# Optimization experiments

Measured on AMD Instinct MI355X. Metric: run time of the kernel, lower is better.

## Reference

```python
import jax, jax.numpy as jnp
import numpy as np

K_MASK = jnp.finfo(jnp.bfloat16).min
ROPE_THETA = 1000000.0


def _rope_sincos(position_ids, head_dim, theta):
    # position_ids: [b, t] int -> sin, cos: [b, t, head_dim//2]
    frac = jnp.arange(0, head_dim, 2, dtype=jnp.float32) / head_dim
    timescale = theta ** frac
    ang = position_ids[..., None].astype(jnp.float32) / timescale
    return jnp.sin(ang), jnp.cos(ang)


def _apply_rope(x, sin, cos):
    # x: [b, t, n, h]; sin/cos: [b, t, h//2]
    h = x.shape[-1]
    x1, x2 = x[..., : h // 2], x[..., h // 2 :]
    s = sin[:, :, None, :]
    c = cos[:, :, None, :]
    return jnp.concatenate([x1 * c - x2 * s, x2 * c + x1 * s], axis=-1).astype(x.dtype)


def setup_inputs() -> dict:
    key = jax.random.key(0)
    ks = jax.random.split(key, 8)
    b, t, S = 8, 16, 8192
    D, N, K, H = 1536, 12, 2, 128
    std = 0.01  # nnx.initializers.normal() default stddev
    return {
        "x": jax.random.normal(ks[0], (b, t, D), jnp.float32),
        "k_cache": jax.random.normal(ks[1], (b, S, K, H), jnp.float32),
        "v_cache": jax.random.normal(ks[2], (b, S, K, H), jnp.float32),
        "wq": jax.random.normal(ks[3], (D, N, H), jnp.float32) * std,
        "bq": jnp.zeros((N, H), jnp.float32),
        "wk": jax.random.normal(ks[4], (D, K, H), jnp.float32) * std,
        "bk": jnp.zeros((K, H), jnp.float32),
        "wv": jax.random.normal(ks[5], (D, K, H), jnp.float32) * std,
        "bv": jnp.zeros((K, H), jnp.float32),
        "wo": jax.random.normal(ks[6], (N, H, D), jnp.float32) * std,
        "segment_ids": jnp.ones((b, t), jnp.int32),
        "start_ind": jnp.zeros((8,), jnp.int32),
        "cur_ind": 4096,
    }


def reference(x, k_cache, v_cache, wq, bq, wk, bk, wv, bv, wo,
              segment_ids, start_ind, cur_ind):
    b, t, D = x.shape
    S = k_cache.shape[1]
    N, H = wq.shape[1], wq.shape[2]
    K = wk.shape[1]
    G = N // K  # n_rep
    scale = H ** -0.5

    # projections with bias
    q = jnp.einsum("btd,dnh->btnh", x, wq) + bq
    kp = jnp.einsum("btd,dkh->btkh", x, wk) + bk
    v = jnp.einsum("btd,dkh->btkh", x, wv) + bv

    # left-pad bookkeeping (count_left_pads) and start index resolution
    nonpad = segment_ids != 0  # [b, t]
    left_pads = jnp.argmax(nonpad, axis=-1).astype(jnp.int32)
    start = jnp.where(start_ind < 0, left_pads, start_ind)  # [b]

    # positions from segment ids, offset by current cache index
    positions = jnp.maximum(jnp.cumsum(nonpad.astype(jnp.int32), axis=-1) - 1, 0) + cur_ind
    sin, cos = _rope_sincos(positions, H, ROPE_THETA)
    q = _apply_rope(q, sin, cos)
    kp = _apply_rope(kp, sin, cos)

    # cache update
    k_cache = jax.lax.dynamic_update_slice(k_cache, kp.astype(k_cache.dtype), (0, cur_ind, 0, 0))
    v_cache = jax.lax.dynamic_update_slice(v_cache, v.astype(v_cache.dtype), (0, cur_ind, 0, 0))

    # GQA attention over full cache
    qg = q.reshape(b, t, K, G, H)
    logits = jnp.einsum("btkgh,bskh->btskg", qg, k_cache) * scale  # [b,t,S,K,G]

    q_pos = cur_ind + jnp.arange(t, dtype=jnp.int32)[None, :] - start[:, None]  # [b,t]
    ts = jnp.arange(S, dtype=jnp.int32)
    kv_seg = (ts[None, :] >= start[:, None]) & (ts[None, :] < cur_ind + t)  # [b,S]
    k_pos = ts[None, :] - start[:, None]
    causal = k_pos[:, None, :] <= q_pos[:, :, None]  # [b,t,S]
    seg = kv_seg[:, None, :].astype(segment_ids.dtype) == segment_ids[:, :, None]  # [b,t,S]
    mask = (causal & seg)[:, :, :, None, None]

    logits = jnp.where(mask, logits, K_MASK)
    w = jax.nn.softmax(logits.astype(jnp.float32), axis=2).astype(logits.dtype)
    qkv = jnp.einsum("btskg,bskh->btkgh", w, v_cache).reshape(b, t, N, H)
    return jnp.einsum("btnh,nhd->btd", qkv, wo)
```

## Files before the change

### kernel.cpp

```cpp
#include <hip/hip_runtime.h>
#include <hip/hip_bf16.h>

#define B_ 8
#define T_ 16
#define D_ 1536
#define N_ 12
#define KH_ 2
#define G_ 6
#define H_ 128
#define S_ 8192
#define NCHUNK 16
#define SPLITS 8

typedef __attribute__((ext_vector_type(8))) short bf16x8;
typedef __attribute__((ext_vector_type(4))) float f32x4;
typedef __attribute__((ext_vector_type(4))) unsigned short u16x4;

__device__ __forceinline__ unsigned short f2bf(float x) {
    unsigned u = __float_as_uint(x);
    u += 0x7fffu + ((u >> 16) & 1u);
    return (unsigned short)(u >> 16);
}
__device__ __forceinline__ float bf2f(unsigned short h) {
    return __uint_as_float(((unsigned)h) << 16);
}

__global__ __launch_bounds__(256, 4) void gemm_splitk(
    const float* __restrict__ A,
    const float* __restrict__ W0, int n0, int ldb0,
    const float* __restrict__ W1, int n1, int ldb1,
    const float* __restrict__ W2, int ldb2,
    float* __restrict__ part, int NTOT, int Kdim)
{
    __shared__ __align__(16) unsigned short Ah[64][40], Al[64][40];
    __shared__ __align__(16) unsigned short Bh[64][40], Bl[64][40];
    const int tid = threadIdx.x;
    const int wave = tid >> 6, lane = tid & 63;
    const int col = lane & 15, g = lane >> 4;
    const int row0 = blockIdx.y * 64;
    const int c0 = blockIdx.x * 64;
    const int ks = Kdim / gridDim.z;
    const int k0 = blockIdx.z * ks;

    const float* Bp; int ldb, bc0;
    if (c0 < n0)           { Bp = W0; ldb = ldb0; bc0 = c0; }
    else if (c0 < n0 + n1) { Bp = W1; ldb = ldb1; bc0 = c0 - n0; }
    else                   { Bp = W2; ldb = ldb2; bc0 = c0 - n0 - n1; }

    f32x4 acc[4];
#pragma unroll
    for (int nt = 0; nt < 4; ++nt) acc[nt] = (f32x4){0.f, 0.f, 0.f, 0.f};

    for (int kk = 0; kk < ks; kk += 32) {
        __syncthreads();
        if (tid < 128) {
#pragma unroll
            for (int c = tid; c < 512; c += 128) {
                int r = c >> 3, k4 = c & 7;
                float4 v = *(const float4*)&A[(size_t)(row0 + r) * Kdim + k0 + kk + k4 * 4];
                float f[4] = {v.x, v.y, v.z, v.w};
                u16x4 hv, lv;
#pragma unroll
                for (int i = 0; i < 4; ++i) {
                    unsigned short hh = f2bf(f[i]);
                    hv[i] = hh; lv[i] = f2bf(f[i] - bf2f(hh));
                }
                *(u16x4*)&Ah[r][k4 * 4] = hv;
                *(u16x4*)&Al[r][k4 * 4] = lv;
            }
        } else {
            int t2 = tid - 128;
            int kq = t2 >> 4, cq = t2 & 15;
            float a[4][4];
#pragma unroll
            for (int r = 0; r < 4; ++r) {
                float4 v = *(const float4*)&Bp[(size_t)(k0 + kk + kq * 4 + r) * ldb + bc0 + cq * 4];
                a[r][0] = v.x; a[r][1] = v.y; a[r][2] = v.z; a[r][3] = v.w;
            }
#pragma unroll
            for (int cc = 0; cc < 4; ++cc) {
                u16x4 hv, lv;
#pragma unroll
                for (int r = 0; r < 4; ++r) {
                    unsigned short hh = f2bf(a[r][cc]);
                    hv[r] = hh; lv[r] = f2bf(a[r][cc] - bf2f(hh));
                }
                *(u16x4*)&Bh[cq * 4 + cc][kq * 4] = hv;
                *(u16x4*)&Bl[cq * 4 + cc][kq * 4] = lv;
            }
        }
        __syncthreads();

        bf16x8 ah = *(const bf16x8*)&Ah[wave * 16 + col][g * 8];
        bf16x8 al = *(const bf16x8*)&Al[wave * 16 + col][g * 8];
#pragma unroll
        for (int nt = 0; nt < 4; ++nt) {
            bf16x8 bh = *(const bf16x8*)&Bh[nt * 16 + col][g * 8];
            bf16x8 bl = *(const bf16x8*)&Bl[nt * 16 + col][g * 8];
            acc[nt] = __builtin_amdgcn_mfma_f32_16x16x32_bf16(ah, bh, acc[nt], 0, 0, 0);
            acc[nt] = __builtin_amdgcn_mfma_f32_16x16x32_bf16(ah, bl, acc[nt], 0, 0, 0);
            acc[nt] = __builtin_amdgcn_mfma_f32_16x16x32_bf16(al, bh, acc[nt], 0, 0, 0);
        }
    }
#pragma unroll
    for (int nt = 0; nt < 4; ++nt)
#pragma unroll
        for (int j = 0; j < 4; ++j) {
            size_t prow = (size_t)blockIdx.z * 128 + row0 + wave * 16 + g * 4 + j;
            part[prow * NTOT + c0 + nt * 16 + col] = acc[nt][j];
        }
}

__global__ __launch_bounds__(256) void rope_reduce(
    const float* __restrict__ part,
    const float* __restrict__ bq, const float* __restrict__ bk,
    const float* __restrict__ bv,
    const int* __restrict__ seg, const int* __restrict__ curp,
    float* __restrict__ q_rope, float* __restrict__ k_new,
    float* __restrict__ v_new)
{
    const int row = blockIdx.x;
    const int b = row >> 4, t = row & 15;
    const int tid = threadIdx.x;
    __shared__ float S[2048];
    __shared__ float sc[64][2];

    const int CUR = curp[0];
    int c = 0;
    for (int tt = 0; tt <= t; ++tt) c += (seg[b * T_ + tt] != 0) ? 1 : 0;
    int pos = max(c - 1, 0) + CUR;

    if (tid < 64) {
        float frac = (2.0f * tid) / (float)H_;
        float ts = expf(frac * logf(1000000.0f));
        float ang = (float)pos / ts;
        sc[tid][0] = sinf(ang);
        sc[tid][1] = cosf(ang);
    }
    for (int e = tid; e < 2048; e += 256) {
        float s = 0.f;
#pragma unroll
        for (int sp = 0; sp < SPLITS; ++sp)
            s += part[((size_t)sp * 128 + row) * 2048 + e];
        S[e] = s;
    }
    __syncthreads();

    for (int e = tid; e < 768; e += 256) {
        int n = e >> 6, i = e & 63;
        float x1 = S[n * 128 + i] + bq[n * 128 + i];
        float x2 = S[n * 128 + i + 64] + bq[n * 128 + i + 64];
        float s = sc[i][0], co = sc[i][1];
        q_rope[(size_t)row * 1536 + n * 128 + i]      = x1 * co - x2 * s;
        q_rope[(size_t)row * 1536 + n * 128 + i + 64] = x2 * co + x1 * s;
    }
    if (tid < 128) {
        int n = tid >> 6, i = tid & 63;
        float x1 = S[1536 + n * 128 + i] + bk[n * 128 + i];
        float x2 = S[1536 + n * 128 + i + 64] + bk[n * 128 + i + 64];
        float s = sc[i][0], co = sc[i][1];
        k_new[(size_t)row * 256 + n * 128 + i]      = x1 * co - x2 * s;
        k_new[(size_t)row * 256 + n * 128 + i + 64] = x2 * co + x1 * s;
    }
    v_new[(size_t)row * 256 + tid] = S[1792 + tid] + bv[tid];
}

__global__ __launch_bounds__(384) void attn_mfma(
    const float* __restrict__ q_rope, const float* __restrict__ k_new,
    const float* __restrict__ v_new,
    const float* __restrict__ k_cache, const float* __restrict__ v_cache,
    const int* __restrict__ seg, const int* __restrict__ start_ind,
    const int* __restrict__ curp,
    float* __restrict__ part)
{
    const int chunk = blockIdx.x, b = blockIdx.y, kh = blockIdx.z;
    const int tid = threadIdx.x;
    const int wave = tid >> 6, lane = tid & 63;
    const int col = lane & 15, g = lane >> 4;
    const float scale = 0.088388347648318447f;
    const float NEG_INF = -__builtin_inff();

    const int CUR = curp[0];
    const int SPAN = CUR + T_;
    const int CH = (SPAN + NCHUNK - 1) / NCHUNK;
    const int s0 = chunk * CH;
    const int s1 = min(s0 + CH, SPAN);

    int st = start_ind[b];
    if (st < 0) {
        st = 0;
        for (int tt = 0; tt < T_; ++tt)
            if (seg[b * T_ + tt] != 0) { st = tt; break; }
    }

    __shared__ __align__(16) unsigned short Vt[6][128][32];
    __shared__ __align__(16) unsigned short Pl[6][16][40];

    const int qbase = wave * 16;
    const int qi_a = qbase + col;
    const int t_a = (qi_a * 171) >> 10;
    const int gh_a = qi_a - t_a * G_;
    const float* qp = &q_rope[(((size_t)b * T_ + t_a) * N_ + kh * G_ + gh_a) * H_];
    bf16x8 qh[4], ql[4];
#pragma unroll
    for (int ks = 0; ks < 4; ++ks) {
        float4 va = *(const float4*)&qp[ks * 32 + g * 8];
        float4 vb = *(const float4*)&qp[ks * 32 + g * 8 + 4];
        float f[8] = {va.x, va.y, va.z, va.w, vb.x, vb.y, vb.z, vb.w};
#pragma unroll
        for (int i = 0; i < 8; ++i) {
            float xs = f[i] * scale;
            unsigned short hh = f2bf(xs);
            qh[ks][i] = (short)hh;
            ql[ks][i] = (short)f2bf(xs - bf2f(hh));
        }
    }

    int qpos_r[4], segid_r[4];
#pragma unroll
    for (int j = 0; j < 4; ++j) {
        int qi_c = qbase + g * 4 + j;
        int t_c = (qi_c * 171) >> 10;
        segid_r[j] = seg[b * T_ + t_c];
        qpos_r[j] = CUR + t_c - st;
    }

    float m[4], lsum[4];
#pragma unroll
    for (int j = 0; j < 4; ++j) { m[j] = NEG_INF; lsum[j] = 0.f; }
    f32x4 oacc[8];
#pragma unroll
    for (int nt = 0; nt < 8; ++nt) oacc[nt] = (f32x4){0.f, 0.f, 0.f, 0.f};

    auto krow = [&](int s) -> const float* {
        s = min(s, SPAN - 1);
        return (s < CUR)
            ? &k_cache[((((size_t)b * S_ + s) * KH_) + kh) * H_]
            : &k_new[((((size_t)b * T_ + (s - CUR)) * KH_) + kh) * H_];
    };
    auto vrow = [&](int s) -> const float* {
        s = min(s, SPAN - 1);
        return (s < CUR)
            ? &v_cache[((((size_t)b * S_ + s) * KH_) + kh) * H_]
            : &v_new[((((size_t)b * T_ + (s - CUR)) * KH_) + kh) * H_];
    };

    auto loadK = [&](float4* kf, int stile) {
#pragma unroll
        for (int kt = 0; kt < 2; ++kt) {
            const float* kr = krow(stile + kt * 16 + col);
#pragma unroll
            for (int ks = 0; ks < 4; ++ks) {
                kf[kt * 8 + ks * 2 + 0] = *(const float4*)(kr + ks * 32 + g * 8);
                kf[kt * 8 + ks * 2 + 1] = *(const float4*)(kr + ks * 32 + g * 8 + 4);
            }
        }
    };
    auto loadV = [&](float4* vf, int stile) {
#pragma unroll
        for (int r = 0; r < 8; ++r) {
            const float* vr = vrow(stile + g * 8 + r);
            vf[r * 2 + 0] = *(const float4*)(vr + col * 8);
            vf[r * 2 + 1] = *(const float4*)(vr + col * 8 + 4);
        }
    };

    const int ntiles = (s1 - s0 + 31) >> 5;
    float4 kf[16], vf[16];
    loadK(kf, s0);

    for (int ti = 0; ti < ntiles; ++ti) {
        const int stile = s0 + ti * 32;
        loadV(vf, stile);

        f32x4 sacc0 = {0.f, 0.f, 0.f, 0.f}, sacc1 = {0.f, 0.f, 0.f, 0.f};
#pragma unroll
        for (int kt = 0; kt < 2; ++kt) {
#pragma unroll
            for (int ks = 0; ks < 4; ++ks) {
                float4 a = kf[kt * 8 + ks * 2], bb = kf[kt * 8 + ks * 2 + 1];
                float f[8] = {a.x, a.y, a.z, a.w, bb.x, bb.y, bb.z, bb.w};
                union { bf16x8 v; __hip_bfloat162 h2[4]; } Hh, Ll;
#pragma unroll
                for (int i = 0; i < 4; ++i) {
                    float2 p = make_float2(f[2 * i], f[2 * i + 1]);
                    Hh.h2[i] = __float22bfloat162_rn(p);
                    float2 q = __bfloat1622float2(Hh.h2[i]);
                    Ll.h2[i] = __float22bfloat162_rn(make_float2(p.x - q.x, p.y - q.y));
                }
                if (kt == 0) {
                    sacc0 = __builtin_amdgcn_mfma_f32_16x16x32_bf16(qh[ks], Hh.v, sacc0, 0, 0, 0);
                    sacc0 = __builtin_amdgcn_mfma_f32_16x16x32_bf16(ql[ks], Hh.v, sacc0, 0, 0, 0);
                    sacc0 = __builtin_amdgcn_mfma_f32_16x16x32_bf16(qh[ks], Ll.v, sacc0, 0, 0, 0);
                } else {
                    sacc1 = __builtin_amdgcn_mfma_f32_16x16x32_bf16(qh[ks], Hh.v, sacc1, 0, 0, 0);
                    sacc1 = __builtin_amdgcn_mfma_f32_16x16x32_bf16(ql[ks], Hh.v, sacc1, 0, 0, 0);
                    sacc1 = __builtin_amdgcn_mfma_f32_16x16x32_bf16(qh[ks], Ll.v, sacc1, 0, 0, 0);
                }
            }
        }

        if (ti + 1 < ntiles) loadK(kf, stile + 32);

        float rj[4];
        const int skey0 = stile + col, skey1 = stile + 16 + col;
#pragma unroll
        for (int j = 0; j < 4; ++j) {
            bool v0 = (skey0 < s1) && (skey0 - st <= qpos_r[j]) &&
                      (((skey0 >= st) ? 1 : 0) == segid_r[j]);
            bool v1 = (skey1 < s1) && (skey1 - st <= qpos_r[j]) &&
                      (((skey1 >= st) ? 1 : 0) == segid_r[j]);
            float lg0 = v0 ? sacc0[j] : NEG_INF;
            float lg1 = v1 ? sacc1[j] : NEG_INF;
            float tm = fmaxf(lg0, lg1);
            tm = fmaxf(tm, __shfl_xor(tm, 1));
            tm = fmaxf(tm, __shfl_xor(tm, 2));
            tm = fmaxf(tm, __shfl_xor(tm, 4));
            tm = fmaxf(tm, __shfl_xor(tm, 8));
            float mn = fmaxf(m[j], tm);
            float r, p0, p1;
            if (mn == NEG_INF) { r = 1.f; p0 = 0.f; p1 = 0.f; }
            else {
                r  = __expf(m[j] - mn);
                p0 = __expf(lg0 - mn);
                p1 = __expf(lg1 - mn);
            }
            float ps = p0 + p1;
            ps += __shfl_xor(ps, 1);
            ps += __shfl_xor(ps, 2);
            ps += __shfl_xor(ps, 4);
            ps += __shfl_xor(ps, 8);
            lsum[j] = lsum[j] * r + ps;
            m[j] = mn;
            rj[j] = r;
            int row = g * 4 + j;
            Pl[wave][row][col]      = f2bf(p0);
            Pl[wave][row][16 + col] = f2bf(p1);
        }

#pragma unroll
        for (int nt = 0; nt < 8; ++nt) {
#pragma unroll
            for (int j = 0; j < 4; ++j) oacc[nt][j] *= rj[j];
        }

#pragma unroll
        for (int c = 0; c < 8; ++c) {
            float fr[8];
#pragma unroll
            for (int r = 0; r < 8; ++r)
                fr[r] = ((const float*)&vf[r * 2 + (c >> 2)])[c & 3];
            union { bf16x8 v; __hip_bfloat162 h2[4]; } W;
#pragma unroll
            for (int i = 0; i < 4; ++i)
                W.h2[i] = __float22bfloat162_rn(make_float2(fr[2 * i], fr[2 * i + 1]));
            *(bf16x8*)&Vt[wave][(c << 4) | col][g * 8] = W.v;
        }

        bf16x8 pa = *(const bf16x8*)&Pl[wave][col][g * 8];
#pragma unroll
        for (int nt = 0; nt < 8; ++nt) {
            bf16x8 vb = *(const bf16x8*)&Vt[wave][((col & 7) << 4) | (nt * 2) | (col >> 3)][g * 8];
            oacc[nt] = __builtin_amdgcn_mfma_f32_16x16x32_bf16(pa, vb, oacc[nt], 0, 0, 0);
        }
    }

    const size_t base_q = (((size_t)chunk * B_ + b) * KH_ + kh) * 96;
#pragma unroll
    for (int j = 0; j < 4; ++j) {
        int qi = qbase + g * 4 + j;
        size_t pb = (base_q + qi) * 132;
        if (col == 0) { part[pb] = m[j]; part[pb + 1] = lsum[j]; }
#pragma unroll
        for (int nt = 0; nt < 8; ++nt)
            part[pb + 2 + nt * 16 + col] = oacc[nt][j];
    }
}

__global__ __launch_bounds__(256) void combine_kernel(
    const float* __restrict__ part, float* __restrict__ qkv)
{
    const int row = blockIdx.x;
    const int b = row >> 4, t = row & 15;
    const int tid = threadIdx.x;
    const int half = tid >> 7, h = tid & 127;
    const size_t cstride = (size_t)B_ * KH_ * 96 * 132;

    for (int nb = 0; nb < N_; nb += 2) {
        int n = nb + half;
        int kh = n / G_, g = n - kh * G_;
        int qi = t * G_ + g;
        size_t base0 = (((size_t)b * KH_ + kh) * 96 + qi) * 132;
        float M = -__builtin_inff();
        for (int c = 0; c < NCHUNK; ++c)
            M = fmaxf(M, part[base0 + c * cstride]);
        float den = 0.f, num = 0.f;
        for (int c = 0; c < NCHUNK; ++c) {
            float mc = part[base0 + c * cstride];
            float e = (M == -__builtin_inff() || mc == -__builtin_inff())
                          ? 0.f : expf(mc - M);
            den += e * part[base0 + c * cstride + 1];
            num += e * part[base0 + c * cstride + 2 + h];
        }
        qkv[(size_t)row * (N_ * H_) + n * H_ + h] = (den > 0.f) ? num / den : 0.f;
    }
}

__global__ __launch_bounds__(256) void sum_reduce(
    const float* __restrict__ part, float* __restrict__ out, int n)
{
    int i = blockIdx.x * 256 + threadIdx.x;
    if (i < n) {
        float s = 0.f;
#pragma unroll
        for (int sp = 0; sp < SPLITS; ++sp) s += part[(size_t)sp * n + i];
        out[i] = s;
    }
}

extern "C" void kernel_launch(void* const* d_in, const int* in_sizes, int n_in,
                              void* d_out, int out_size, void* d_ws, size_t ws_size,
                              hipStream_t stream)
{
    (void)in_sizes; (void)n_in; (void)out_size; (void)ws_size;
    const float* x       = (const float*)d_in[0];
    const float* k_cache = (const float*)d_in[1];
    const float* v_cache = (const float*)d_in[2];
    const float* wq      = (const float*)d_in[3];
    const float* bq      = (const float*)d_in[4];
    const float* wk      = (const float*)d_in[5];
    const float* bk      = (const float*)d_in[6];
    const float* wv      = (const float*)d_in[7];
    const float* bv      = (const float*)d_in[8];
    const float* wo      = (const float*)d_in[9];
    const int*   seg     = (const int*)d_in[10];
    const int*   start_i = (const int*)d_in[11];
    const int*   curp    = (const int*)d_in[12];
    float* out = (float*)d_out;
    float* ws  = (float*)d_ws;

    const size_t PSZ  = (size_t)NCHUNK * B_ * KH_ * 96 * 132;
    const size_t QSZ  = (size_t)B_ * T_ * N_ * H_;
    const size_t KSZ  = (size_t)B_ * T_ * KH_ * H_;
    float* partP  = ws;
    float* partA  = ws;
    float* q_rope = ws + PSZ;
    float* k_new  = q_rope + QSZ;
    float* v_new  = k_new + KSZ;
    float* qkv    = v_new + KSZ;

    gemm_splitk<<<dim3(32, 2, SPLITS), 256, 0, stream>>>(
        x, wq, 1536, 1536, wk, 256, 256, wv, 256, partP, 2048, D_);

    rope_reduce<<<B_ * T_, 256, 0, stream>>>(partP, bq, bk, bv, seg, curp,
                                             q_rope, k_new, v_new);

    attn_mfma<<<dim3(NCHUNK, B_, KH_), 384, 0, stream>>>(
        q_rope, k_new, v_new, k_cache, v_cache, seg, start_i, curp, partA);

    combine_kernel<<<B_ * T_, 256, 0, stream>>>(partA, qkv);

    gemm_splitk<<<dim3(24, 2, SPLITS), 256, 0, stream>>>(
        qkv, wo, 1536, 1536, wo, 0, 1536, wo, 1536, partP, 1536, N_ * H_);

    sum_reduce<<<(B_ * T_ * D_ + 255) / 256, 256, 0, stream>>>(
        partP, out, B_ * T_ * D_);
}
```

Before: 98.80 us.

## Stage K/V tiles in shared LDS with double buffering, single-pass bf16 QK

```diff
diff --git a/kernel.cpp b/kernel.cpp
--- a/kernel.cpp
+++ b/kernel.cpp
@@ -25,6 +25,13 @@
     return __uint_as_float(((unsigned)h) << 16);
 }
 
+__device__ __forceinline__ void gload16(const float* g, void* l) {
+    __builtin_amdgcn_global_load_lds(
+        (const __attribute__((address_space(1))) unsigned int*)g,
+        (__attribute__((address_space(3))) unsigned int*)l,
+        16, 0, 0);
+}
+
 __global__ __launch_bounds__(256, 4) void gemm_splitk(
     const float* __restrict__ A,
     const float* __restrict__ W0, int n0, int ldb0,
@@ -165,7 +172,7 @@
     v_new[(size_t)row * 256 + tid] = S[1792 + tid] + bv[tid];
 }
 
-__global__ __launch_bounds__(384) void attn_mfma(
+__global__ __launch_bounds__(384, 3) void attn_mfma(
     const float* __restrict__ q_rope, const float* __restrict__ k_new,
     const float* __restrict__ v_new,
     const float* __restrict__ k_cache, const float* __restrict__ v_cache,
@@ -193,7 +200,8 @@
             if (seg[b * T_ + tt] != 0) { st = tt; break; }
     }
 
-    __shared__ __align__(16) unsigned short Vt[6][128][32];
+    __shared__ __align__(16) float Ksw[2][32][128];
+    __shared__ __align__(16) unsigned short Vt[2][128][40];
     __shared__ __align__(16) unsigned short Pl[6][16][40];
 
     const int qbase = wave * 16;
@@ -201,19 +209,17 @@
     const int t_a = (qi_a * 171) >> 10;
     const int gh_a = qi_a - t_a * G_;
     const float* qp = &q_rope[(((size_t)b * T_ + t_a) * N_ + kh * G_ + gh_a) * H_];
-    bf16x8 qh[4], ql[4];
+    bf16x8 qf[4];
 #pragma unroll
     for (int ks = 0; ks < 4; ++ks) {
         float4 va = *(const float4*)&qp[ks * 32 + g * 8];
         float4 vb = *(const float4*)&qp[ks * 32 + g * 8 + 4];
         float f[8] = {va.x, va.y, va.z, va.w, vb.x, vb.y, vb.z, vb.w};
-#pragma unroll
-        for (int i = 0; i < 8; ++i) {
-            float xs = f[i] * scale;
-            unsigned short hh = f2bf(xs);
-            qh[ks][i] = (short)hh;
-            ql[ks][i] = (short)f2bf(xs - bf2f(hh));
-        }
+        union { bf16x8 v; __hip_bfloat162 h2[4]; } W;
+#pragma unroll
+        for (int i = 0; i < 4; ++i)
+            W.h2[i] = __float22bfloat162_rn(make_float2(f[2 * i] * scale, f[2 * i + 1] * scale));
+        qf[ks] = W.v;
     }
 
     int qpos_r[4], segid_r[4];
@@ -245,62 +251,65 @@
             : &v_new[((((size_t)b * T_ + (s - CUR)) * KH_) + kh) * H_];
     };
 
-    auto loadK = [&](float4* kf, int stile) {
+    auto stageK = [&](int bufi, int stile) {
+#pragma unroll
+        for (int i = 0; i < 3; ++i) {
+            int idx = tid + i * 384;
+            if (idx < 1024) {
+                int row = idx >> 5, s = idx & 31;
+                int sg = s ^ (row & 7);
+                gload16(krow(stile + row) + sg * 4, &Ksw[bufi][row][s * 4]);
+            }
+        }
+    };
+    const int vky4 = tid >> 5, vd4 = tid & 31;
+    auto loadV = [&](float4* vreg, int stile) {
+        if (tid < 256) {
+#pragma unroll
+            for (int r = 0; r < 4; ++r)
+                vreg[r] = *(const float4*)(vrow(stile + vky4 * 4 + r) + vd4 * 4);
+        }
+    };
+    auto writeV = [&](int bufi, const float4* vreg) {
+        if (tid < 256) {
+            float a[4][4];
+#pragma unroll
+            for (int r = 0; r < 4; ++r) {
+                a[r][0] = vreg[r].x; a[r][1] = vreg[r].y;
+                a[r][2] = vreg[r].z; a[r][3] = vreg[r].w;
+            }
+#pragma unroll
+            for (int dd = 0; dd < 4; ++dd) {
+                u16x4 hv;
+#pragma unroll
+                for (int r = 0; r < 4; ++r) hv[r] = f2bf(a[r][dd]);
+                *(u16x4*)&Vt[bufi][vd4 * 4 + dd][vky4 * 4] = hv;
+            }
+        }
+    };
+
+    auto computeTile = [&](int bufi, int stile) {
+        f32x4 sacc0 = {0.f, 0.f, 0.f, 0.f}, sacc1 = {0.f, 0.f, 0.f, 0.f};
 #pragma unroll
         for (int kt = 0; kt < 2; ++kt) {
-            const float* kr = krow(stile + kt * 16 + col);
+            const int row = kt * 16 + col;
+            const int rx = row & 7;
 #pragma unroll
             for (int ks = 0; ks < 4; ++ks) {
-                kf[kt * 8 + ks * 2 + 0] = *(const float4*)(kr + ks * 32 + g * 8);
-                kf[kt * 8 + ks * 2 + 1] = *(const float4*)(kr + ks * 32 + g * 8 + 4);
-            }
-        }
-    };
-    auto loadV = [&](float4* vf, int stile) {
-#pragma unroll
-        for (int r = 0; r < 8; ++r) {
-            const float* vr = vrow(stile + g * 8 + r);
-            vf[r * 2 + 0] = *(const float4*)(vr + col * 8);
-            vf[r * 2 + 1] = *(const float4*)(vr + col * 8 + 4);
-        }
-    };
-
-    const int ntiles = (s1 - s0 + 31) >> 5;
-    float4 kf[16], vf[16];
-    loadK(kf, s0);
-
-    for (int ti = 0; ti < ntiles; ++ti) {
-        const int stile = s0 + ti * 32;
-        loadV(vf, stile);
-
-        f32x4 sacc0 = {0.f, 0.f, 0.f, 0.f}, sacc1 = {0.f, 0.f, 0.f, 0.f};
-#pragma unroll
-        for (int kt = 0; kt < 2; ++kt) {
-#pragma unroll
-            for (int ks = 0; ks < 4; ++ks) {
-                float4 a = kf[kt * 8 + ks * 2], bb = kf[kt * 8 + ks * 2 + 1];
+                const int sl = ks * 8 + g * 2;
+                float4 a = *(const float4*)&Ksw[bufi][row][(sl ^ rx) * 4];
+                float4 bb = *(const float4*)&Ksw[bufi][row][((sl + 1) ^ rx) * 4];
                 float f[8] = {a.x, a.y, a.z, a.w, bb.x, bb.y, bb.z, bb.w};
-                union { bf16x8 v; __hip_bfloat162 h2[4]; } Hh, Ll;
-#pragma unroll
-                for (int i = 0; i < 4; ++i) {
-                    float2 p = make_float2(f[2 * i], f[2 * i + 1]);
-                    Hh.h2[i] = __float22bfloat162_rn(p);
-                    float2 q = __bfloat1622float2(Hh.h2[i]);
-                    Ll.h2[i] = __float22bfloat162_rn(make_float2(p.x - q.x, p.y - q.y));
-                }
-                if (kt == 0) {
-                    sacc0 = __builtin_amdgcn_mfma_f32_16x16x32_bf16(qh[ks], Hh.v, sacc0, 0, 0, 0);
-                    sacc0 = __builtin_amdgcn_mfma_f32_16x16x32_bf16(ql[ks], Hh.v, sacc0, 0, 0, 0);
-                    sacc0 = __builtin_amdgcn_mfma_f32_16x16x32_bf16(qh[ks], Ll.v, sacc0, 0, 0, 0);
-                } else {
-                    sacc1 = __builtin_amdgcn_mfma_f32_16x16x32_bf16(qh[ks], Hh.v, sacc1, 0, 0, 0);
-                    sacc1 = __builtin_amdgcn_mfma_f32_16x16x32_bf16(ql[ks], Hh.v, sacc1, 0, 0, 0);
-                    sacc1 = __builtin_amdgcn_mfma_f32_16x16x32_bf16(qh[ks], Ll.v, sacc1, 0, 0, 0);
-                }
-            }
-        }
-
-        if (ti + 1 < ntiles) loadK(kf, stile + 32);
+                union { bf16x8 v; __hip_bfloat162 h2[4]; } W;
+#pragma unroll
+                for (int i = 0; i < 4; ++i)
+                    W.h2[i] = __float22bfloat162_rn(make_float2(f[2 * i], f[2 * i + 1]));
+                if (kt == 0)
+                    sacc0 = __builtin_amdgcn_mfma_f32_16x16x32_bf16(qf[ks], W.v, sacc0, 0, 0, 0);
+                else
+                    sacc1 = __builtin_amdgcn_mfma_f32_16x16x32_bf16(qf[ks], W.v, sacc1, 0, 0, 0);
+            }
+        }
 
         float rj[4];
         const int skey0 = stile + col, skey1 = stile + 16 + col;
@@ -344,24 +353,31 @@
             for (int j = 0; j < 4; ++j) oacc[nt][j] *= rj[j];
         }
 
-#pragma unroll
-        for (int c = 0; c < 8; ++c) {
-            float fr[8];
-#pragma unroll
-            for (int r = 0; r < 8; ++r)
-                fr[r] = ((const float*)&vf[r * 2 + (c >> 2)])[c & 3];
-            union { bf16x8 v; __hip_bfloat162 h2[4]; } W;
-#pragma unroll
-            for (int i = 0; i < 4; ++i)
-                W.h2[i] = __float22bfloat162_rn(make_float2(fr[2 * i], fr[2 * i + 1]));
-            *(bf16x8*)&Vt[wave][(c << 4) | col][g * 8] = W.v;
-        }
-
         bf16x8 pa = *(const bf16x8*)&Pl[wave][col][g * 8];
 #pragma unroll
         for (int nt = 0; nt < 8; ++nt) {
-            bf16x8 vb = *(const bf16x8*)&Vt[wave][((col & 7) << 4) | (nt * 2) | (col >> 3)][g * 8];
+            bf16x8 vb = *(const bf16x8*)&Vt[bufi][nt * 16 + col][g * 8];
             oacc[nt] = __builtin_amdgcn_mfma_f32_16x16x32_bf16(pa, vb, oacc[nt], 0, 0, 0);
+        }
+    };
+
+    const int ntiles = (s1 - s0 + 31) >> 5;
+    float4 vA[4], vB[4];
+    stageK(0, s0);
+    loadV(vA, s0);
+    writeV(0, vA);
+    __syncthreads();
+
+    for (int ti = 0; ti < ntiles; ti += 2) {
+        if (ti + 1 < ntiles) { stageK(1, s0 + (ti + 1) * 32); loadV(vB, s0 + (ti + 1) * 32); }
+        computeTile(0, s0 + ti * 32);
+        if (ti + 1 < ntiles) writeV(1, vB);
+        __syncthreads();
+        if (ti + 1 < ntiles) {
+            if (ti + 2 < ntiles) { stageK(0, s0 + (ti + 2) * 32); loadV(vA, s0 + (ti + 2) * 32); }
+            computeTile(1, s0 + (ti + 1) * 32);
+            if (ti + 2 < ntiles) writeV(0, vA);
+            __syncthreads();
         }
     }
 
```

Result: faster. 96.49 us (-2.3%).
